# Optimization experiments

Measured on AMD Instinct MI355X. Metric: run time of the kernel, lower is better.

The kernel has to match this reference:

```python
import jax, jax.numpy as jnp
import numpy as np

EPS = 1e-8

def _normalize(a):
    return a / jnp.clip(jnp.linalg.norm(a, axis=-1, keepdims=True), EPS)

def _cosine(a, b):
    # pairwise cosine similarity: [Na, d] x [Nb, d] -> [Na, Nb]
    return _normalize(a) @ _normalize(b).T

def setup_inputs() -> dict:
    key = jax.random.key(0)
    n, k, q, d = 100, 5, 75, 4096
    x = jax.random.normal(key, (n * (k + q), d), dtype=jnp.float32)
    tao = jnp.full((1,), 10.0, dtype=jnp.float32)
    return {"x": x, "tao": tao, "n": n, "k": k, "q": q}

def reference(x, tao, n, k, q):
    d = x.shape[-1]
    x = x.reshape(n, k + q, d)
    support = x[:, :k]                      # [n, k, d]
    query = x[:, k:].reshape(n * q, d)      # [NQ, d]
    NQ = n * q
    proto = support.mean(axis=1)            # [n, d]

    pre_sim = _cosine(query, proto)         # [NQ, n]
    pre_label = jnp.argmax(pre_sim, axis=1) # [NQ]

    # vectorized per-class masked softmax aggregation (replaces Python loop)
    cls_ids = jnp.arange(n)
    mask = pre_label[None, :] == cls_ids[:, None]            # [n, NQ]
    logits_q = jnp.where(mask, pre_sim.T, -jnp.inf)          # [n, NQ]
    proto_n = _normalize(proto)
    self_sim = jnp.sum(proto_n * proto_n, axis=-1)           # [n], cosine(proto, proto)
    logits = jnp.concatenate([logits_q, self_sim[:, None]], axis=1)  # [n, NQ+1]
    w = jax.nn.softmax(logits, axis=1)                       # [n, NQ+1]
    adapted_proto = w[:, :NQ] @ query + w[:, NQ:] * proto    # [n, d]

    sim = _cosine(query, adapted_proto)                      # [NQ, n]
    return tao.reshape(()) * sim
```

## Files before the change

### kernel.cpp

```cpp
#include <hip/hip_runtime.h>
#include <hip/hip_bf16.h>
#include <math.h>

#define NQUERY 7500
#define NCLS   100
#define DIM    4096
#define KQ     75
#define KSUP   5
#define RPC    80
#define MPAD   7552
#define NPAD   112
#define CAPQ   256
#define RCAP   2048
#define EPSF   1e-8f
#define SELEM  845824
#define SLICE_BYTES 3383296u

typedef __attribute__((ext_vector_type(8))) short bf16x8;
typedef __attribute__((ext_vector_type(4))) short s16x4;
typedef __attribute__((ext_vector_type(4))) float f32x4;

__device__ __forceinline__ int xrow_of_query(int j) {
    return (j / KQ) * RPC + KSUP + (j % KQ);
}
__device__ __forceinline__ short bf16t(float x) {
    union { float f; unsigned u; } v; v.f = x;
    return (short)(v.u >> 16);
}

__device__ __forceinline__ size_t tile_off(int nt, int lm, int i) {
    return (((size_t)(nt * 128 + (i >> 5)) * 4 + ((i >> 3) & 3)) * 16 + lm) * 8 + (i & 7);
}

__global__ __launch_bounds__(256) void k_proto(const float* __restrict__ x,
        float* __restrict__ proto, short* __restrict__ Phi, float* __restrict__ es,
        double* __restrict__ pninv) {
    const int c = blockIdx.x, t = threadIdx.x;
    const int nt = c >> 4, lm = c & 15;
    if (c >= NCLS) {
        for (int g = t; g < 512; g += 256) {
            const int kstep = g >> 2, kq = g & 3;
            size_t o = (((size_t)(nt * 128 + kstep) * 4 + kq) * 16 + lm) * 8;
            bf16x8 z = {0,0,0,0,0,0,0,0};
            *(bf16x8*)(Phi + o) = z;
        }
        if (t == 0) es[c] = 0.f;
        return;
    }
    __shared__ double red[4];
    __shared__ float s_inv;
    const float* b0 = x + (size_t)(c * RPC) * DIM;
    float v[16];
    double ssq = 0.0;
#pragma unroll
    for (int p = 0; p < 4; ++p) {
        const int i = p * 1024 + t * 4;
        f32x4 s = {0.f, 0.f, 0.f, 0.f};
#pragma unroll
        for (int r = 0; r < KSUP; ++r)
            s += *(const f32x4*)(b0 + (size_t)r * DIM + i);
        s = s / 5.0f;
        *(f32x4*)&v[p*4] = s;
        *(f32x4*)(proto + (size_t)c*DIM + i) = s;
        ssq += (double)s[0]*s[0] + (double)s[1]*s[1]
             + (double)s[2]*s[2] + (double)s[3]*s[3];
    }
    for (int o = 32; o; o >>= 1) ssq += __shfl_down(ssq, o);
    if ((t & 63) == 0) red[t >> 6] = ssq;
    __syncthreads();
    if (t == 0) {
        double dtot = red[0] + red[1] + red[2] + red[3];
        pninv[c] = 1.0 / sqrt(dtot);
        float tot = (float)dtot;
        float inv = 1.f / fmaxf(sqrtf(tot), EPSF);
        s_inv = inv;
        es[c] = expf(tot * inv * inv);
    }
    __syncthreads();
    const float inv = s_inv;
#pragma unroll
    for (int p = 0; p < 4; ++p) {
        const int i = p * 1024 + t * 4;
        s16x4 h;
#pragma unroll
        for (int e = 0; e < 4; ++e) h[e] = bf16t(v[p*4+e] * inv);
        *(s16x4*)(Phi + tile_off(nt, lm, i)) = h;
    }
}

template<int TNKS, bool SSQ>
__global__ __launch_bounds__(256, 4) void k_gemm(const float* __restrict__ x,
        const short* __restrict__ Bt, float* __restrict__ Part, float* __restrict__ nq2) {
    constexpr int KST = 128 / TNKS;
    const int bx = blockIdx.x, kz = blockIdx.y;
    const int w = threadIdx.x >> 6, lane = threadIdx.x & 63;
    const int lm = lane & 15, kq = lane >> 4;
    const int mt = bx * 4 + w;
    const int j = mt * 16 + lm;
    const int jc = j < NQUERY ? j : NQUERY - 1;
    const float* pa = x + (size_t)xrow_of_query(jc) * DIM + kq * 8;
    const short* pb = Bt + (lane << 3);
    const int ks0 = kz * KST;

    f32x4 acc[7];
#pragma unroll
    for (int nt = 0; nt < 7; ++nt) acc[nt] = (f32x4){0.f,0.f,0.f,0.f};
    float ssq = 0.f;

#pragma unroll 1
    for (int cc = 0; cc < KST / 8; ++cc) {
#pragma unroll
        for (int u = 0; u < 8; ++u) {
            const int ks = ks0 + cc * 8 + u;
            const f32x4 a0 = *(const f32x4*)(pa + (size_t)ks * 32);
            const f32x4 a1 = *(const f32x4*)(pa + (size_t)ks * 32 + 4);
            bf16x8 bh[7];
#pragma unroll
            for (int nt = 0; nt < 7; ++nt)
                bh[nt] = *(const bf16x8*)(pb + (((size_t)(nt * 128 + ks)) << 9));
            float fv[8] = {a0[0],a0[1],a0[2],a0[3],a1[0],a1[1],a1[2],a1[3]};
            bf16x8 ah;
#pragma unroll
            for (int e = 0; e < 8; ++e) {
                if (SSQ) ssq += fv[e] * fv[e];
                ah[e] = bf16t(fv[e]);
            }
#pragma unroll
            for (int nt = 0; nt < 7; ++nt)
                acc[nt] = __builtin_amdgcn_mfma_f32_16x16x32_bf16(ah, bh[nt], acc[nt], 0, 0, 0);
        }
    }

    if (SSQ) {
        float s2 = ssq;
        s2 += __shfl_xor(s2, 16);
        s2 += __shfl_xor(s2, 32);
        if (kq == 0 && j < NQUERY) atomicAdd(&nq2[j], s2);
    }
    float* sp = Part + (size_t)kz * SELEM + (size_t)(mt * 16) * NPAD;
#pragma unroll
    for (int nt = 0; nt < 7; ++nt)
#pragma unroll
        for (int r = 0; r < 4; ++r)
            sp[(size_t)(kq * 4 + r) * NPAD + nt * 16 + lm] = acc[nt][r];
}

__global__ __launch_bounds__(256) void k_reduce1(const float* __restrict__ Spart,
        float* __restrict__ Sred, int nks) {
    const int idx = blockIdx.x * 256 + threadIdx.x;
    const size_t e = (size_t)idx * 4;
    f32x4 s = {0.f, 0.f, 0.f, 0.f};
    for (int kz = 0; kz < nks; ++kz)
        s += *(const f32x4*)(Spart + (size_t)kz * SELEM + e);
    *(f32x4*)(Sred + e) = s;
}

__global__ __launch_bounds__(256) void k_argmax(const float* __restrict__ S,
        const float* __restrict__ nq2, float* __restrict__ coef, float* __restrict__ invq,
        int* __restrict__ pos, int* __restrict__ ccnt, int* __restrict__ cls_list,
        int* __restrict__ rcnt, int* __restrict__ rlist) {
    const int j = blockIdx.x * 256 + threadIdx.x;
    if (j >= NQUERY) return;
    const float* row = S + (size_t)j * NPAD;
    float m1 = -1e30f, m2 = -1e30f;
    int i1 = 0, i2 = 0;
    for (int c = 0; c < NCLS; ++c) {
        float v = row[c];
        if (v > m1) { m2 = m1; i2 = i1; m1 = v; i1 = c; }
        else if (v > m2) { m2 = v; i2 = c; }
    }
    const float inv = 1.f / fmaxf(sqrtf(nq2[j]), EPSF);
    invq[j] = inv;
    coef[j] = expf(m1 * inv);
    const int p = atomicAdd(&ccnt[i1], 1);
    if (p < CAPQ) { cls_list[i1 * CAPQ + p] = j; pos[j] = p; }
    else pos[j] = -1;
    if ((m1 - m2) * inv < 5e-4f) {
        int rp = atomicAdd(rcnt, 1);
        if (rp < RCAP) rlist[rp] = j | (i1 << 13) | (i2 << 20);
    }
}

__global__ __launch_bounds__(256) void k_refine(const float* __restrict__ x,
        const float* __restrict__ proto, const double* __restrict__ pninv,
        const float* __restrict__ S, const float* __restrict__ invq,
        float* __restrict__ coef, const int* __restrict__ pos,
        int* __restrict__ ccnt, int* __restrict__ cls_list,
        const int* __restrict__ rcnt, const int* __restrict__ rlist) {
    const int cnt = min(*rcnt, RCAP);
    const int t = threadIdx.x;
    __shared__ double red1[4], red2[4];
    for (int e = blockIdx.x; e < cnt; e += gridDim.x) {
        const int pk = rlist[e];
        const int j = pk & 8191, c1 = (pk >> 13) & 127, c2 = (pk >> 20) & 127;
        const float* xq = x + (size_t)xrow_of_query(j) * DIM;
        const float* p1 = proto + (size_t)c1 * DIM;
        const float* p2 = proto + (size_t)c2 * DIM;
        double d1 = 0.0, d2 = 0.0;
        for (int i = t; i < DIM; i += 256) {
            const double qv = (double)xq[i];
            d1 += (double)p1[i] * qv;
            d2 += (double)p2[i] * qv;
        }
        for (int o = 32; o; o >>= 1) { d1 += __shfl_down(d1, o); d2 += __shfl_down(d2, o); }
        if ((t & 63) == 0) { red1[t >> 6] = d1; red2[t >> 6] = d2; }
        __syncthreads();
        if (t == 0) {
            const double cos1 = (red1[0]+red1[1]+red1[2]+red1[3]) * pninv[c1];
            const double cos2 = (red2[0]+red2[1]+red2[2]+red2[3]) * pninv[c2];
            const int win = (cos2 > cos1 || (cos2 == cos1 && c2 < c1)) ? c2 : c1;
            if (win != c1) {
                coef[j] = expf(S[(size_t)j * NPAD + win] * invq[j]);
                const int pj = pos[j];
                if (pj >= 0) cls_list[c1 * CAPQ + pj] = -1;
                const int np = atomicAdd(&ccnt[c2], 1);
                if (np < CAPQ) cls_list[c2 * CAPQ + np] = j;
            }
        }
        __syncthreads();
    }
}

__global__ __launch_bounds__(128) void k_adapt(const float* __restrict__ x,
        const float* __restrict__ coef, const int* __restrict__ cls_cnt,
        const int* __restrict__ cls_list, float* __restrict__ APpart) {
    __shared__ int   s_j[CAPQ];
    __shared__ float s_cf[CAPQ];
    const int cx = blockIdx.x, c = blockIdx.y, sl = blockIdx.z;
    const int n = min(cls_cnt[c], CAPQ);
    for (int e = threadIdx.x; e < n; e += 128) {
        const int j = cls_list[c * CAPQ + e];
        s_j[e] = j;
        s_cf[e] = (j >= 0) ? coef[j] : 0.f;
    }
    __syncthreads();
    const int i0 = cx * 512 + threadIdx.x * 4;
    f32x4 acc = {0.f, 0.f, 0.f, 0.f};
    for (int e = sl; e < n; e += 4) {
        const int j = s_j[e];
        if (j >= 0) {
            const float cf = s_cf[e];
            const f32x4 v = *(const f32x4*)(x + (size_t)xrow_of_query(j) * DIM + i0);
            acc += v * cf;
        }
    }
    *(f32x4*)(APpart + (size_t)sl * NCLS * DIM + (size_t)c * DIM + i0) = acc;
}

__global__ __launch_bounds__(256) void k_apnorm(const float* __restrict__ APpart,
        const float* __restrict__ proto, const float* __restrict__ es,
        short* __restrict__ APhi) {
    const int c = blockIdx.x, t = threadIdx.x;
    const int nt = c >> 4, lm = c & 15;
    if (c >= NCLS) {
        for (int g = t; g < 512; g += 256) {
            const int kstep = g >> 2, kq = g & 3;
            size_t o = (((size_t)(nt * 128 + kstep) * 4 + kq) * 16 + lm) * 8;
            bf16x8 z = {0,0,0,0,0,0,0,0};
            *(bf16x8*)(APhi + o) = z;
        }
        return;
    }
    __shared__ float red[4];
    __shared__ float s_inv;
    const float e0 = es[c];
    float v[16];
    float ssq = 0.f;
#pragma unroll
    for (int p = 0; p < 4; ++p) {
        const int i = p * 1024 + t * 4;
        f32x4 s = {0.f, 0.f, 0.f, 0.f};
#pragma unroll
        for (int sl = 0; sl < 4; ++sl)
            s += *(const f32x4*)(APpart + (size_t)sl * NCLS * DIM + (size_t)c * DIM + i);
        f32x4 pr = *(const f32x4*)(proto + (size_t)c*DIM + i);
        s += pr * e0;
        *(f32x4*)&v[p*4] = s;
        ssq += s[0]*s[0] + s[1]*s[1] + s[2]*s[2] + s[3]*s[3];
    }
    for (int o = 32; o; o >>= 1) ssq += __shfl_down(ssq, o);
    if ((t & 63) == 0) red[t >> 6] = ssq;
    __syncthreads();
    if (t == 0) {
        float tot = red[0] + red[1] + red[2] + red[3];
        s_inv = 1.f / fmaxf(sqrtf(tot), EPSF);
    }
    __syncthreads();
    const float inv = s_inv;
#pragma unroll
    for (int p = 0; p < 4; ++p) {
        const int i = p * 1024 + t * 4;
        s16x4 h;
#pragma unroll
        for (int e = 0; e < 4; ++e) h[e] = bf16t(v[p*4+e] * inv);
        *(s16x4*)(APhi + tile_off(nt, lm, i)) = h;
    }
}

__global__ __launch_bounds__(256) void k_reduce2(const float* __restrict__ Opart,
        const float* __restrict__ invq, const float* __restrict__ tao,
        float* __restrict__ out, int nks) {
    const int idx = blockIdx.x * 256 + threadIdx.x;
    if (idx >= NQUERY * 25) return;
    const int j = idx / 25, c4 = (idx % 25) * 4;
    const size_t e = (size_t)j * NPAD + c4;
    f32x4 s = {0.f, 0.f, 0.f, 0.f};
    for (int kz = 0; kz < nks; ++kz)
        s += *(const f32x4*)(Opart + (size_t)kz * SELEM + e);
    const float sc = tao[0] * invq[j];
    *(f32x4*)(out + (size_t)j * NCLS + c4) = s * sc;
}

#define OFF_RCNT   0u
#define OFF_CCNT   256u
#define OFF_NQ2    1792u
#define ZERO_BYTES 32768u
#define OFF_ES     32768u
#define OFF_INVQ   33280u
#define OFF_POS    63488u
#define OFF_COEF   93696u
#define OFF_RLIST  123904u
#define OFF_CLIST  132096u
#define OFF_PNINV  234496u
#define OFF_PROTO  235520u
#define OFF_PHI    1873920u
#define OFF_APHI   2791424u
#define OFF_SRED   3708928u
#define OFF_APPART 7092224u
#define OFF_PART   13645824u

extern "C" void kernel_launch(void* const* d_in, const int* in_sizes, int n_in,
                              void* d_out, int out_size, void* d_ws, size_t ws_size,
                              hipStream_t stream) {
    const float* x   = (const float*)d_in[0];
    const float* tao = (const float*)d_in[1];
    char* ws = (char*)d_ws;

    int*    rcnt    = (int*)   (ws + OFF_RCNT);
    int*    ccnt    = (int*)   (ws + OFF_CCNT);
    float*  nq2     = (float*) (ws + OFF_NQ2);
    float*  es      = (float*) (ws + OFF_ES);
    float*  invq    = (float*) (ws + OFF_INVQ);
    int*    pos     = (int*)   (ws + OFF_POS);
    float*  coef    = (float*) (ws + OFF_COEF);
    int*    rlist   = (int*)   (ws + OFF_RLIST);
    int*    clist   = (int*)   (ws + OFF_CLIST);
    double* pninv   = (double*)(ws + OFF_PNINV);
    float*  proto   = (float*) (ws + OFF_PROTO);
    short*  Phi     = (short*) (ws + OFF_PHI);
    short*  APhi    = (short*) (ws + OFF_APHI);
    float*  Sred    = (float*) (ws + OFF_SRED);
    float*  APpart  = (float*) (ws + OFF_APPART);
    float*  Part    = (float*) (ws + OFF_PART);

    int nks = 1;
    if (ws_size > (size_t)OFF_PART + SLICE_BYTES) {
        size_t avail = (ws_size - OFF_PART) / SLICE_BYTES;
        nks = avail >= 16 ? 16 : (int)avail;
        while (nks & (nks - 1)) nks &= nks - 1;
    }

    hipMemsetAsync(ws, 0, ZERO_BYTES, stream);

    k_proto <<<NPAD, 256, 0, stream>>>(x, proto, Phi, es, pninv);
    switch (nks) {
        case 16: k_gemm<16,true><<<dim3(118, 16), 256, 0, stream>>>(x, Phi, Part, nq2); break;
        case 8:  k_gemm<8, true><<<dim3(118, 8),  256, 0, stream>>>(x, Phi, Part, nq2); break;
        case 4:  k_gemm<4, true><<<dim3(118, 4),  256, 0, stream>>>(x, Phi, Part, nq2); break;
        case 2:  k_gemm<2, true><<<dim3(118, 2),  256, 0, stream>>>(x, Phi, Part, nq2); break;
        default: k_gemm<1, true><<<dim3(118, 1),  256, 0, stream>>>(x, Phi, Part, nq2); break;
    }
    k_reduce1<<<826, 256, 0, stream>>>(Part, Sred, nks);
    k_argmax <<<30, 256, 0, stream>>>(Sred, nq2, coef, invq, pos, ccnt, clist, rcnt, rlist);
    k_refine <<<512, 256, 0, stream>>>(x, proto, pninv, Sred, invq, coef, pos, ccnt, clist, rcnt, rlist);
    k_adapt  <<<dim3(8, NCLS, 4), 128, 0, stream>>>(x, coef, ccnt, clist, APpart);
    k_apnorm <<<NPAD, 256, 0, stream>>>(APpart, proto, es, APhi);
    switch (nks) {
        case 16: k_gemm<16,false><<<dim3(118, 16), 256, 0, stream>>>(x, APhi, Part, nq2); break;
        case 8:  k_gemm<8, false><<<dim3(118, 8),  256, 0, stream>>>(x, APhi, Part, nq2); break;
        case 4:  k_gemm<4, false><<<dim3(118, 4),  256, 0, stream>>>(x, APhi, Part, nq2); break;
        case 2:  k_gemm<2, false><<<dim3(118, 2),  256, 0, stream>>>(x, APhi, Part, nq2); break;
        default: k_gemm<1, false><<<dim3(118, 1),  256, 0, stream>>>(x, APhi, Part, nq2); break;
    }
    k_reduce2<<<733, 256, 0, stream>>>(Part, invq, tao, (float*)d_out, nks);
}
```

Before: 338.2 us.

## Use atomic split-K accumulation and two M-tiles per wave in GEMMs

Each wave now computes two 16-row query tiles, so every B fragment load feeds two MFMAs. The A loads are software-prefetched one k-step ahead. Split-K partial slices and the separate reduce kernels are replaced by float atomicAdd directly into the zeroed result buffers, with split-K fixed at 16 instead of sized from the workspace. This removes the partial-buffer write/read traffic and one kernel launch per GEMM, at the cost of many atomics, lower occupancy (launch bounds 3), an extra memset, and nondeterministic summation order that could flip argmax ties.

```diff
diff --git a/kernel.cpp b/kernel.cpp
--- a/kernel.cpp
+++ b/kernel.cpp
@@ -14,7 +14,6 @@
 #define RCAP   2048
 #define EPSF   1e-8f
 #define SELEM  845824
-#define SLICE_BYTES 3383296u
 
 typedef __attribute__((ext_vector_type(8))) short bf16x8;
 typedef __attribute__((ext_vector_type(4))) short s16x4;
@@ -89,70 +88,83 @@
 }
 
 template<int TNKS, bool SSQ>
-__global__ __launch_bounds__(256, 4) void k_gemm(const float* __restrict__ x,
-        const short* __restrict__ Bt, float* __restrict__ Part, float* __restrict__ nq2) {
+__global__ __launch_bounds__(256, 3) void k_gemm(const float* __restrict__ x,
+        const short* __restrict__ Bt, float* __restrict__ Sd, float* __restrict__ nq2) {
     constexpr int KST = 128 / TNKS;
     const int bx = blockIdx.x, kz = blockIdx.y;
     const int w = threadIdx.x >> 6, lane = threadIdx.x & 63;
     const int lm = lane & 15, kq = lane >> 4;
-    const int mt = bx * 4 + w;
-    const int j = mt * 16 + lm;
-    const int jc = j < NQUERY ? j : NQUERY - 1;
-    const float* pa = x + (size_t)xrow_of_query(jc) * DIM + kq * 8;
+    const int mp = bx * 4 + w;
+    const int mt0 = mp * 2, mt1 = mt0 + 1;
+    const int j0 = mt0 * 16 + lm, j1 = mt1 * 16 + lm;
+    const int jc0 = j0 < NQUERY ? j0 : NQUERY - 1;
+    const int jc1 = j1 < NQUERY ? j1 : NQUERY - 1;
+    const float* pa0 = x + (size_t)xrow_of_query(jc0) * DIM + kq * 8;
+    const float* pa1 = x + (size_t)xrow_of_query(jc1) * DIM + kq * 8;
     const short* pb = Bt + (lane << 3);
     const int ks0 = kz * KST;
 
-    f32x4 acc[7];
-#pragma unroll
-    for (int nt = 0; nt < 7; ++nt) acc[nt] = (f32x4){0.f,0.f,0.f,0.f};
-    float ssq = 0.f;
+    f32x4 acc0[7], acc1[7];
+#pragma unroll
+    for (int nt = 0; nt < 7; ++nt) {
+        acc0[nt] = (f32x4){0.f,0.f,0.f,0.f};
+        acc1[nt] = (f32x4){0.f,0.f,0.f,0.f};
+    }
+    float ssq0 = 0.f, ssq1 = 0.f;
+
+    f32x4 a00 = *(const f32x4*)(pa0 + (size_t)ks0 * 32);
+    f32x4 a01 = *(const f32x4*)(pa0 + (size_t)ks0 * 32 + 4);
+    f32x4 a10 = *(const f32x4*)(pa1 + (size_t)ks0 * 32);
+    f32x4 a11 = *(const f32x4*)(pa1 + (size_t)ks0 * 32 + 4);
 
 #pragma unroll 1
-    for (int cc = 0; cc < KST / 8; ++cc) {
-#pragma unroll
-        for (int u = 0; u < 8; ++u) {
-            const int ks = ks0 + cc * 8 + u;
-            const f32x4 a0 = *(const f32x4*)(pa + (size_t)ks * 32);
-            const f32x4 a1 = *(const f32x4*)(pa + (size_t)ks * 32 + 4);
-            bf16x8 bh[7];
-#pragma unroll
-            for (int nt = 0; nt < 7; ++nt)
-                bh[nt] = *(const bf16x8*)(pb + (((size_t)(nt * 128 + ks)) << 9));
-            float fv[8] = {a0[0],a0[1],a0[2],a0[3],a1[0],a1[1],a1[2],a1[3]};
-            bf16x8 ah;
-#pragma unroll
-            for (int e = 0; e < 8; ++e) {
-                if (SSQ) ssq += fv[e] * fv[e];
-                ah[e] = bf16t(fv[e]);
-            }
-#pragma unroll
-            for (int nt = 0; nt < 7; ++nt)
-                acc[nt] = __builtin_amdgcn_mfma_f32_16x16x32_bf16(ah, bh[nt], acc[nt], 0, 0, 0);
-        }
+    for (int s = 0; s < KST; ++s) {
+        const int ks = ks0 + s;
+        bf16x8 bh[7];
+#pragma unroll
+        for (int nt = 0; nt < 7; ++nt)
+            bh[nt] = *(const bf16x8*)(pb + (((size_t)(nt * 128 + ks)) << 9));
+        f32x4 n00, n01, n10, n11;
+        if (s + 1 < KST) {
+            n00 = *(const f32x4*)(pa0 + (size_t)(ks + 1) * 32);
+            n01 = *(const f32x4*)(pa0 + (size_t)(ks + 1) * 32 + 4);
+            n10 = *(const f32x4*)(pa1 + (size_t)(ks + 1) * 32);
+            n11 = *(const f32x4*)(pa1 + (size_t)(ks + 1) * 32 + 4);
+        }
+        float f0[8] = {a00[0],a00[1],a00[2],a00[3],a01[0],a01[1],a01[2],a01[3]};
+        float f1[8] = {a10[0],a10[1],a10[2],a10[3],a11[0],a11[1],a11[2],a11[3]};
+        bf16x8 ah0, ah1;
+#pragma unroll
+        for (int e = 0; e < 8; ++e) {
+            if (SSQ) { ssq0 += f0[e] * f0[e]; ssq1 += f1[e] * f1[e]; }
+            ah0[e] = bf16t(f0[e]);
+            ah1[e] = bf16t(f1[e]);
+        }
+#pragma unroll
+        for (int nt = 0; nt < 7; ++nt) {
+            acc0[nt] = __builtin_amdgcn_mfma_f32_16x16x32_bf16(ah0, bh[nt], acc0[nt], 0, 0, 0);
+            acc1[nt] = __builtin_amdgcn_mfma_f32_16x16x32_bf16(ah1, bh[nt], acc1[nt], 0, 0, 0);
+        }
+        a00 = n00; a01 = n01; a10 = n10; a11 = n11;
     }
 
     if (SSQ) {
-        float s2 = ssq;
-        s2 += __shfl_xor(s2, 16);
-        s2 += __shfl_xor(s2, 32);
-        if (kq == 0 && j < NQUERY) atomicAdd(&nq2[j], s2);
-    }
-    float* sp = Part + (size_t)kz * SELEM + (size_t)(mt * 16) * NPAD;
+        ssq0 += __shfl_xor(ssq0, 16); ssq0 += __shfl_xor(ssq0, 32);
+        ssq1 += __shfl_xor(ssq1, 16); ssq1 += __shfl_xor(ssq1, 32);
+        if (kq == 0) {
+            if (j0 < NQUERY) atomicAdd(&nq2[j0], ssq0);
+            if (j1 < NQUERY) atomicAdd(&nq2[j1], ssq1);
+        }
+    }
+    float* s0 = Sd + (size_t)(mt0 * 16) * NPAD;
+    float* s1 = Sd + (size_t)(mt1 * 16) * NPAD;
 #pragma unroll
     for (int nt = 0; nt < 7; ++nt)
 #pragma unroll
-        for (int r = 0; r < 4; ++r)
-            sp[(size_t)(kq * 4 + r) * NPAD + nt * 16 + lm] = acc[nt][r];
-}
-
-__global__ __launch_bounds__(256) void k_reduce1(const float* __restrict__ Spart,
-        float* __restrict__ Sred, int nks) {
-    const int idx = blockIdx.x * 256 + threadIdx.x;
-    const size_t e = (size_t)idx * 4;
-    f32x4 s = {0.f, 0.f, 0.f, 0.f};
-    for (int kz = 0; kz < nks; ++kz)
-        s += *(const f32x4*)(Spart + (size_t)kz * SELEM + e);
-    *(f32x4*)(Sred + e) = s;
+        for (int r = 0; r < 4; ++r) {
+            atomicAdd(&s0[(size_t)(kq * 4 + r) * NPAD + nt * 16 + lm], acc0[nt][r]);
+            atomicAdd(&s1[(size_t)(kq * 4 + r) * NPAD + nt * 16 + lm], acc1[nt][r]);
+        }
 }
 
 __global__ __launch_bounds__(256) void k_argmax(const float* __restrict__ S,
@@ -297,16 +309,13 @@
     }
 }
 
-__global__ __launch_bounds__(256) void k_reduce2(const float* __restrict__ Opart,
+__global__ __launch_bounds__(256) void k_scale(const float* __restrict__ Ored,
         const float* __restrict__ invq, const float* __restrict__ tao,
-        float* __restrict__ out, int nks) {
+        float* __restrict__ out) {
     const int idx = blockIdx.x * 256 + threadIdx.x;
     if (idx >= NQUERY * 25) return;
     const int j = idx / 25, c4 = (idx % 25) * 4;
-    const size_t e = (size_t)j * NPAD + c4;
-    f32x4 s = {0.f, 0.f, 0.f, 0.f};
-    for (int kz = 0; kz < nks; ++kz)
-        s += *(const f32x4*)(Opart + (size_t)kz * SELEM + e);
+    const f32x4 s = *(const f32x4*)(Ored + (size_t)j * NPAD + c4);
     const float sc = tao[0] * invq[j];
     *(f32x4*)(out + (size_t)j * NCLS + c4) = s * sc;
 }
@@ -326,8 +335,8 @@
 #define OFF_PHI    1873920u
 #define OFF_APHI   2791424u
 #define OFF_SRED   3708928u
-#define OFF_APPART 7092224u
-#define OFF_PART   13645824u
+#define OFF_ORED   7092224u
+#define OFF_APPART 10475520u
 
 extern "C" void kernel_launch(void* const* d_in, const int* in_sizes, int n_in,
                               void* d_out, int out_size, void* d_ws, size_t ws_size,
@@ -350,37 +359,18 @@
     short*  Phi     = (short*) (ws + OFF_PHI);
     short*  APhi    = (short*) (ws + OFF_APHI);
     float*  Sred    = (float*) (ws + OFF_SRED);
+    float*  Ored    = (float*) (ws + OFF_ORED);
     float*  APpart  = (float*) (ws + OFF_APPART);
-    float*  Part    = (float*) (ws + OFF_PART);
-
-    int nks = 1;
-    if (ws_size > (size_t)OFF_PART + SLICE_BYTES) {
-        size_t avail = (ws_size - OFF_PART) / SLICE_BYTES;
-        nks = avail >= 16 ? 16 : (int)avail;
-        while (nks & (nks - 1)) nks &= nks - 1;
-    }
 
     hipMemsetAsync(ws, 0, ZERO_BYTES, stream);
+    hipMemsetAsync(ws + OFF_SRED, 0, 2u * 3383296u, stream);
 
     k_proto <<<NPAD, 256, 0, stream>>>(x, proto, Phi, es, pninv);
-    switch (nks) {
-        case 16: k_gemm<16,true><<<dim3(118, 16), 256, 0, stream>>>(x, Phi, Part, nq2); break;
-        case 8:  k_gemm<8, true><<<dim3(118, 8),  256, 0, stream>>>(x, Phi, Part, nq2); break;
-        case 4:  k_gemm<4, true><<<dim3(118, 4),  256, 0, stream>>>(x, Phi, Part, nq2); break;
-        case 2:  k_gemm<2, true><<<dim3(118, 2),  256, 0, stream>>>(x, Phi, Part, nq2); break;
-        default: k_gemm<1, true><<<dim3(118, 1),  256, 0, stream>>>(x, Phi, Part, nq2); break;
-    }
-    k_reduce1<<<826, 256, 0, stream>>>(Part, Sred, nks);
+    k_gemm<16, true><<<dim3(59, 16), 256, 0, stream>>>(x, Phi, Sred, nq2);
     k_argmax <<<30, 256, 0, stream>>>(Sred, nq2, coef, invq, pos, ccnt, clist, rcnt, rlist);
     k_refine <<<512, 256, 0, stream>>>(x, proto, pninv, Sred, invq, coef, pos, ccnt, clist, rcnt, rlist);
     k_adapt  <<<dim3(8, NCLS, 4), 128, 0, stream>>>(x, coef, ccnt, clist, APpart);
     k_apnorm <<<NPAD, 256, 0, stream>>>(APpart, proto, es, APhi);
-    switch (nks) {
-        case 16: k_gemm<16,false><<<dim3(118, 16), 256, 0, stream>>>(x, APhi, Part, nq2); break;
-        case 8:  k_gemm<8, false><<<dim3(118, 8),  256, 0, stream>>>(x, APhi, Part, nq2); break;
-        case 4:  k_gemm<4, false><<<dim3(118, 4),  256, 0, stream>>>(x, APhi, Part, nq2); break;
-        case 2:  k_gemm<2, false><<<dim3(118, 2),  256, 0, stream>>>(x, APhi, Part, nq2); break;
-        default: k_gemm<1, false><<<dim3(118, 1),  256, 0, stream>>>(x, APhi, Part, nq2); break;
-    }
-    k_reduce2<<<733, 256, 0, stream>>>(Part, invq, tao, (float*)d_out, nks);
-}
+    k_gemm<16, false><<<dim3(59, 16), 256, 0, stream>>>(x, APhi, Ored, nq2);
+    k_scale  <<<733, 256, 0, stream>>>(Ored, invq, tao, (float*)d_out);
+}
```

New measurement: 358.6 us. 1.06x slower.
